# Kernel optimization log

Hardware: AMD Instinct MI355X
Metric: run time of the kernel (lower is better)

## Reference

```python
import jax, jax.numpy as jnp
import numpy as np

BLOCK_SIZE = 16
# Signed NVFP4 (e2m1) value table; code = sign_bit<<3 | magnitude_index
FP4_VALUES = jnp.array(
    [0.0, 0.5, 1.0, 1.5, 2.0, 3.0, 4.0, 6.0,
     -0.0, -0.5, -1.0, -1.5, -2.0, -3.0, -4.0, -6.0],
    dtype=jnp.float32)


def setup_inputs() -> dict:
    key = jax.random.key(0)
    k1, k2, k3 = jax.random.split(key, 3)
    O, I = 4096, 4096
    x = jax.random.normal(k1, (2, 1024, I), dtype=jnp.float32)
    # per-block scales (positive), one per 16-element block along in_features
    weight_scales = jax.random.uniform(k2, (O, I // BLOCK_SIZE), dtype=jnp.float32,
                                       minval=0.01, maxval=1.0)
    weight_q = jax.random.randint(k3, (O, I), 0, 16, dtype=jnp.int32)
    return {"x": x, "weight_scales": weight_scales, "weight_q": weight_q}


def dequantize_nvfp4_sim(weight_q, weight_scales, block_size=BLOCK_SIZE):
    O, I = weight_q.shape
    vals = FP4_VALUES[weight_q]                              # [O, I] fp32 e2m1 values
    w = vals.reshape(O, I // block_size, block_size) * weight_scales[:, :, None]
    return w.reshape(O, I)


def reference(x, weight_scales, weight_q):
    # Dequantize NVFP4 -> BF16, then BF16 GEMM (F.linear), cast back to input dtype.
    w = dequantize_nvfp4_sim(weight_q, weight_scales).astype(jnp.bfloat16)  # [O, I]
    x_bf16 = x.astype(jnp.bfloat16)
    out = jnp.einsum('bsi,oi->bso', x_bf16, w)               # [B, S, O] bf16
    return out.astype(x.dtype)
```

## Files before the change

kernel.cpp:

```cpp
#include <hip/hip_runtime.h>

typedef __bf16  bf16x8 __attribute__((ext_vector_type(8)));
typedef float   f32x4  __attribute__((ext_vector_type(4)));
typedef short   short8 __attribute__((ext_vector_type(8)));

static __device__ __forceinline__ unsigned short f2bf(float f) {
  union { float f; unsigned int u; } v; v.f = f;
  unsigned int u = v.u;
  u += 0x7fffu + ((u >> 16) & 1u);
  return (unsigned short)(u >> 16);
}

static __device__ __forceinline__ float fp4_decode(int qc) {
  int e = (qc >> 1) & 3;
  float m = (float)(qc & 1);
  float mag = (e == 0) ? (0.5f * m)
                       : ((2.0f + m) * 0.5f * (float)(1 << (e - 1)));
  return (qc & 8) ? -mag : mag;
}

__global__ __launch_bounds__(256) void w4a16_dequant_w(
    const int* __restrict__ wq, const float* __restrict__ wsc,
    short* __restrict__ wout, int nblk) {
  int idx = blockIdx.x * 256 + threadIdx.x;
  if (idx >= nblk) return;
  float s = wsc[idx];
  const int4* qp = (const int4*)wq + (size_t)idx * 4;
  int4 q0 = qp[0], q1 = qp[1], q2 = qp[2], q3 = qp[3];
  short8 r0, r1;
  r0[0] = (short)f2bf(fp4_decode(q0.x) * s);
  r0[1] = (short)f2bf(fp4_decode(q0.y) * s);
  r0[2] = (short)f2bf(fp4_decode(q0.z) * s);
  r0[3] = (short)f2bf(fp4_decode(q0.w) * s);
  r0[4] = (short)f2bf(fp4_decode(q1.x) * s);
  r0[5] = (short)f2bf(fp4_decode(q1.y) * s);
  r0[6] = (short)f2bf(fp4_decode(q1.z) * s);
  r0[7] = (short)f2bf(fp4_decode(q1.w) * s);
  r1[0] = (short)f2bf(fp4_decode(q2.x) * s);
  r1[1] = (short)f2bf(fp4_decode(q2.y) * s);
  r1[2] = (short)f2bf(fp4_decode(q2.z) * s);
  r1[3] = (short)f2bf(fp4_decode(q2.w) * s);
  r1[4] = (short)f2bf(fp4_decode(q3.x) * s);
  r1[5] = (short)f2bf(fp4_decode(q3.y) * s);
  r1[6] = (short)f2bf(fp4_decode(q3.z) * s);
  r1[7] = (short)f2bf(fp4_decode(q3.w) * s);
  short8* op = (short8*)wout + (size_t)idx * 2;
  op[0] = r0;
  op[1] = r1;
}

__global__ __launch_bounds__(256) void w4a16_convert_x(
    const float* __restrict__ x, short* __restrict__ xb, int n8) {
  int idx = blockIdx.x * 256 + threadIdx.x;
  if (idx >= n8) return;
  const float4* xp = (const float4*)x + (size_t)idx * 2;
  float4 a = xp[0], b = xp[1];
  short8 r;
  r[0] = (short)f2bf(a.x); r[1] = (short)f2bf(a.y);
  r[2] = (short)f2bf(a.z); r[3] = (short)f2bf(a.w);
  r[4] = (short)f2bf(b.x); r[5] = (short)f2bf(b.y);
  r[6] = (short)f2bf(b.z); r[7] = (short)f2bf(b.w);
  ((short8*)xb)[idx] = r;
}

#define BM 128
#define BN 256
#define BK 64
#define NBUF 3
#define ASZ (BM * BK)
#define BSZ (BN * BK)

__global__ __launch_bounds__(512, 2) void w4a16_gemm_2ph(
    const short* __restrict__ A, const short* __restrict__ B,
    float* __restrict__ C, int M, int N, int K) {
  __shared__ __attribute__((aligned(16))) short As[NBUF * ASZ];
  __shared__ __attribute__((aligned(16))) short Bs[NBUF * BSZ];

  const int tid  = threadIdx.x;
  const int lane = tid & 63;
  const int wid  = tid >> 6;
  const int wr   = wid >> 2;
  const int wc   = wid & 3;

  const int bm = blockIdx.y * BM;
  const int bn = blockIdx.x * BN;

  f32x4 acc[4][4] = {};

  const int fr    = lane & 15;
  const int klane = lane >> 4;
  const int xv    = fr & 7;

  const size_t rowbytes = (size_t)K * 2;

  size_t aoff[2];  int aldso[2];
#pragma unroll
  for (int r = 0; r < 2; ++r) {
    int u = r * 512 + tid;
    int row = u >> 3, c = u & 7;
    int csrc = c ^ (row & 7);
    aoff[r]  = (size_t)(bm + row) * rowbytes + (size_t)csrc * 16;
    aldso[r] = u * 16;
  }
  size_t boff[4];  int bldso[4];
#pragma unroll
  for (int r = 0; r < 4; ++r) {
    int u = r * 512 + tid;
    int row = u >> 3, c = u & 7;
    int csrc = c ^ (row & 7);
    boff[r]  = (size_t)(bn + row) * rowbytes + (size_t)csrc * 16;
    bldso[r] = u * 16;
  }

  const char* Ag = (const char*)A;
  const char* Bg = (const char*)B;

#define STAGE_A(bufbase, koff2, r)                                              \
  __builtin_amdgcn_global_load_lds(                                             \
      (const __attribute__((address_space(1))) unsigned int*)(Ag + aoff[r] + (koff2)), \
      (__attribute__((address_space(3))) unsigned int*)((char*)(bufbase) + aldso[r]),  \
      16, 0, 0)
#define STAGE_B(bufbase, koff2, r)                                              \
  __builtin_amdgcn_global_load_lds(                                             \
      (const __attribute__((address_space(1))) unsigned int*)(Bg + boff[r] + (koff2)), \
      (__attribute__((address_space(3))) unsigned int*)((char*)(bufbase) + bldso[r]),  \
      16, 0, 0)

  auto readA = [&](const short* Ab, int mq, int mi, int kk) -> bf16x8 {
    int row = wr * 64 + mq * 32 + mi * 16 + fr;
    int c = kk * 4 + klane;
    return *(const bf16x8*)((const char*)Ab + (size_t)row * 128 + ((c ^ xv) << 4));
  };
  auto readB = [&](const short* Bb, int ni, int kk) -> bf16x8 {
    int row = wc * 64 + ni * 16 + fr;
    int c = kk * 4 + klane;
    return *(const bf16x8*)((const char*)Bb + (size_t)row * 128 + ((c ^ xv) << 4));
  };

  const int NT = K / BK;

  {
    char* A0 = (char*)As; char* B0 = (char*)Bs;
    char* A1 = (char*)(As + ASZ); char* B1 = (char*)(Bs + BSZ);
    STAGE_A(A0, 0, 0); STAGE_A(A0, 0, 1);
    STAGE_B(B0, 0, 0); STAGE_B(B0, 0, 1); STAGE_B(B0, 0, 2); STAGE_B(B0, 0, 3);
    size_t k2 = (size_t)BK * 2;
    STAGE_A(A1, k2, 0); STAGE_A(A1, k2, 1);
    STAGE_B(B1, k2, 0); STAGE_B(B1, k2, 1); STAGE_B(B1, k2, 2); STAGE_B(B1, k2, 3);
  }
  asm volatile("s_waitcnt vmcnt(6)");
  __builtin_amdgcn_s_barrier();

  int cur = 0, nxt = 2;
  for (int t = 0; t < NT; ++t) {
    const short* Ab = As + cur * ASZ;
    const short* Bb = Bs + cur * BSZ;
    char* An = (char*)(As + nxt * ASZ);
    char* Bn = (char*)(Bs + nxt * BSZ);
    const size_t koff2 = (size_t)(t + 2) * (BK * 2);
    const bool pf = (t + 2) < NT;

    bf16x8 af[2][2], bfr[4][2];

#pragma unroll
    for (int mi = 0; mi < 2; ++mi)
#pragma unroll
      for (int kk = 0; kk < 2; ++kk)
        af[mi][kk] = readA(Ab, 0, mi, kk);
#pragma unroll
    for (int ni = 0; ni < 4; ++ni)
#pragma unroll
      for (int kk = 0; kk < 2; ++kk)
        bfr[ni][kk] = readB(Bb, ni, kk);

    if (pf) { STAGE_A(An, koff2, 0); STAGE_A(An, koff2, 1); STAGE_B(Bn, koff2, 0); }

    __builtin_amdgcn_s_barrier();
    asm volatile("s_waitcnt lgkmcnt(0)");
    __builtin_amdgcn_s_setprio(1);
#pragma unroll
    for (int mi = 0; mi < 2; ++mi)
#pragma unroll
      for (int ni = 0; ni < 4; ++ni)
#pragma unroll
        for (int kk = 0; kk < 2; ++kk)
          acc[mi][ni] = __builtin_amdgcn_mfma_f32_16x16x32_bf16(
              af[mi][kk], bfr[ni][kk], acc[mi][ni], 0, 0, 0);
    __builtin_amdgcn_s_setprio(0);
    __builtin_amdgcn_s_barrier();

#pragma unroll
    for (int mi = 0; mi < 2; ++mi)
#pragma unroll
      for (int kk = 0; kk < 2; ++kk)
        af[mi][kk] = readA(Ab, 1, mi, kk);

    if (pf) { STAGE_B(Bn, koff2, 1); STAGE_B(Bn, koff2, 2); STAGE_B(Bn, koff2, 3); }

    __builtin_amdgcn_s_barrier();
    asm volatile("s_waitcnt lgkmcnt(0)");
    __builtin_amdgcn_s_setprio(1);
#pragma unroll
    for (int mi = 0; mi < 2; ++mi)
#pragma unroll
      for (int ni = 0; ni < 4; ++ni)
#pragma unroll
        for (int kk = 0; kk < 2; ++kk)
          acc[2 + mi][ni] = __builtin_amdgcn_mfma_f32_16x16x32_bf16(
              af[mi][kk], bfr[ni][kk], acc[2 + mi][ni], 0, 0, 0);
    __builtin_amdgcn_s_setprio(0);

    if (t < NT - 1) {
      if (pf) asm volatile("s_waitcnt vmcnt(6)");
      else    asm volatile("s_waitcnt vmcnt(0)");
    }
    __builtin_amdgcn_s_barrier();

    cur = (cur == NBUF - 1) ? 0 : cur + 1;
    nxt = (nxt == NBUF - 1) ? 0 : nxt + 1;
  }

  const int cn = lane & 15;
  const int rb = (lane >> 4) * 4;
#pragma unroll
  for (int ai = 0; ai < 4; ++ai)
#pragma unroll
    for (int bj = 0; bj < 4; ++bj) {
      int m0 = bm + wr * 64 + ai * 16 + rb;
      int n0 = bn + wc * 64 + bj * 16 + cn;
#pragma unroll
      for (int r = 0; r < 4; ++r)
        C[(size_t)(m0 + r) * N + n0] = acc[ai][bj][r];
    }
}

extern "C" void kernel_launch(void* const* d_in, const int* in_sizes, int n_in,
                              void* d_out, int out_size, void* d_ws, size_t ws_size,
                              hipStream_t stream) {
  const float* x   = (const float*)d_in[0];
  const float* wsc = (const float*)d_in[1];
  const int*   wq  = (const int*)d_in[2];
  float* out = (float*)d_out;

  const int K = 4096;
  const int N = in_sizes[2] / K;
  const int M = in_sizes[0] / K;

  short* Wb = (short*)d_ws;
  short* Xb = Wb + (size_t)N * K;

  int nblk = (N * K) / 16;
  w4a16_dequant_w<<<nblk / 256, 256, 0, stream>>>(wq, wsc, Wb, nblk);
  int n8 = (M * K) / 8;
  w4a16_convert_x<<<n8 / 256, 256, 0, stream>>>(x, Xb, n8);

  dim3 grid(N / BN, M / BM);
  w4a16_gemm_2ph<<<grid, 512, 0, stream>>>(Xb, Wb, out, M, N, K);
}
```

Baseline: 97.93 us.

## Merge prep kernels and collapse GEMM inner loop into one phase

The weight-dequant and activation-convert kernels become a single launch that splits its blocks by index range, removing one launch and the gap between kernels. In the GEMM, the two half-iteration phases are merged: all A and B fragments for the tile are read from LDS up front, all six prefetch loads are issued together, and the two intermediate barriers and lgkmcnt waits are dropped, leaving one barrier per K step. This cuts synchronisation overhead but raises register pressure from the extra A fragments. It also relies on the triple-buffer distance and the end-of-iteration barrier to keep LDS reads and writes from racing.

New measurement: 90.93 us. -7.2%, faster.

```diff
diff --git a/kernel.cpp b/kernel.cpp
--- a/kernel.cpp
+++ b/kernel.cpp
@@ -19,48 +19,49 @@
   return (qc & 8) ? -mag : mag;
 }
 
-__global__ __launch_bounds__(256) void w4a16_dequant_w(
+__global__ __launch_bounds__(256) void w4a16_prep(
     const int* __restrict__ wq, const float* __restrict__ wsc,
-    short* __restrict__ wout, int nblk) {
-  int idx = blockIdx.x * 256 + threadIdx.x;
-  if (idx >= nblk) return;
-  float s = wsc[idx];
-  const int4* qp = (const int4*)wq + (size_t)idx * 4;
-  int4 q0 = qp[0], q1 = qp[1], q2 = qp[2], q3 = qp[3];
-  short8 r0, r1;
-  r0[0] = (short)f2bf(fp4_decode(q0.x) * s);
-  r0[1] = (short)f2bf(fp4_decode(q0.y) * s);
-  r0[2] = (short)f2bf(fp4_decode(q0.z) * s);
-  r0[3] = (short)f2bf(fp4_decode(q0.w) * s);
-  r0[4] = (short)f2bf(fp4_decode(q1.x) * s);
-  r0[5] = (short)f2bf(fp4_decode(q1.y) * s);
-  r0[6] = (short)f2bf(fp4_decode(q1.z) * s);
-  r0[7] = (short)f2bf(fp4_decode(q1.w) * s);
-  r1[0] = (short)f2bf(fp4_decode(q2.x) * s);
-  r1[1] = (short)f2bf(fp4_decode(q2.y) * s);
-  r1[2] = (short)f2bf(fp4_decode(q2.z) * s);
-  r1[3] = (short)f2bf(fp4_decode(q2.w) * s);
-  r1[4] = (short)f2bf(fp4_decode(q3.x) * s);
-  r1[5] = (short)f2bf(fp4_decode(q3.y) * s);
-  r1[6] = (short)f2bf(fp4_decode(q3.z) * s);
-  r1[7] = (short)f2bf(fp4_decode(q3.w) * s);
-  short8* op = (short8*)wout + (size_t)idx * 2;
-  op[0] = r0;
-  op[1] = r1;
-}
-
-__global__ __launch_bounds__(256) void w4a16_convert_x(
+    short* __restrict__ wout, int nblkW,
     const float* __restrict__ x, short* __restrict__ xb, int n8) {
-  int idx = blockIdx.x * 256 + threadIdx.x;
-  if (idx >= n8) return;
-  const float4* xp = (const float4*)x + (size_t)idx * 2;
-  float4 a = xp[0], b = xp[1];
-  short8 r;
-  r[0] = (short)f2bf(a.x); r[1] = (short)f2bf(a.y);
-  r[2] = (short)f2bf(a.z); r[3] = (short)f2bf(a.w);
-  r[4] = (short)f2bf(b.x); r[5] = (short)f2bf(b.y);
-  r[6] = (short)f2bf(b.z); r[7] = (short)f2bf(b.w);
-  ((short8*)xb)[idx] = r;
+  const int nbW = nblkW >> 8;
+  if ((int)blockIdx.x < nbW) {
+    int idx = blockIdx.x * 256 + threadIdx.x;
+    if (idx >= nblkW) return;
+    float s = wsc[idx];
+    const int4* qp = (const int4*)wq + (size_t)idx * 4;
+    int4 q0 = qp[0], q1 = qp[1], q2 = qp[2], q3 = qp[3];
+    short8 r0, r1;
+    r0[0] = (short)f2bf(fp4_decode(q0.x) * s);
+    r0[1] = (short)f2bf(fp4_decode(q0.y) * s);
+    r0[2] = (short)f2bf(fp4_decode(q0.z) * s);
+    r0[3] = (short)f2bf(fp4_decode(q0.w) * s);
+    r0[4] = (short)f2bf(fp4_decode(q1.x) * s);
+    r0[5] = (short)f2bf(fp4_decode(q1.y) * s);
+    r0[6] = (short)f2bf(fp4_decode(q1.z) * s);
+    r0[7] = (short)f2bf(fp4_decode(q1.w) * s);
+    r1[0] = (short)f2bf(fp4_decode(q2.x) * s);
+    r1[1] = (short)f2bf(fp4_decode(q2.y) * s);
+    r1[2] = (short)f2bf(fp4_decode(q2.z) * s);
+    r1[3] = (short)f2bf(fp4_decode(q2.w) * s);
+    r1[4] = (short)f2bf(fp4_decode(q3.x) * s);
+    r1[5] = (short)f2bf(fp4_decode(q3.y) * s);
+    r1[6] = (short)f2bf(fp4_decode(q3.z) * s);
+    r1[7] = (short)f2bf(fp4_decode(q3.w) * s);
+    short8* op = (short8*)wout + (size_t)idx * 2;
+    op[0] = r0;
+    op[1] = r1;
+  } else {
+    int idx = (blockIdx.x - nbW) * 256 + threadIdx.x;
+    if (idx >= n8) return;
+    const float4* xp = (const float4*)x + (size_t)idx * 2;
+    float4 a = xp[0], b = xp[1];
+    short8 r;
+    r[0] = (short)f2bf(a.x); r[1] = (short)f2bf(a.y);
+    r[2] = (short)f2bf(a.z); r[3] = (short)f2bf(a.w);
+    r[4] = (short)f2bf(b.x); r[5] = (short)f2bf(b.y);
+    r[6] = (short)f2bf(b.z); r[7] = (short)f2bf(b.w);
+    ((short8*)xb)[idx] = r;
+  }
 }
 
 #define BM 128
@@ -70,7 +71,7 @@
 #define ASZ (BM * BK)
 #define BSZ (BN * BK)
 
-__global__ __launch_bounds__(512, 2) void w4a16_gemm_2ph(
+__global__ __launch_bounds__(512, 2) void w4a16_gemm_1ph(
     const short* __restrict__ A, const short* __restrict__ B,
     float* __restrict__ C, int M, int N, int K) {
   __shared__ __attribute__((aligned(16))) short As[NBUF * ASZ];
@@ -160,23 +161,30 @@
     const size_t koff2 = (size_t)(t + 2) * (BK * 2);
     const bool pf = (t + 2) < NT;
 
-    bf16x8 af[2][2], bfr[4][2];
+    bf16x8 af0[2][2], bfr[4][2], af1[2][2];
 
 #pragma unroll
     for (int mi = 0; mi < 2; ++mi)
 #pragma unroll
       for (int kk = 0; kk < 2; ++kk)
-        af[mi][kk] = readA(Ab, 0, mi, kk);
+        af0[mi][kk] = readA(Ab, 0, mi, kk);
 #pragma unroll
     for (int ni = 0; ni < 4; ++ni)
 #pragma unroll
       for (int kk = 0; kk < 2; ++kk)
         bfr[ni][kk] = readB(Bb, ni, kk);
-
-    if (pf) { STAGE_A(An, koff2, 0); STAGE_A(An, koff2, 1); STAGE_B(Bn, koff2, 0); }
-
-    __builtin_amdgcn_s_barrier();
-    asm volatile("s_waitcnt lgkmcnt(0)");
+#pragma unroll
+    for (int mi = 0; mi < 2; ++mi)
+#pragma unroll
+      for (int kk = 0; kk < 2; ++kk)
+        af1[mi][kk] = readA(Ab, 1, mi, kk);
+
+    if (pf) {
+      STAGE_A(An, koff2, 0); STAGE_A(An, koff2, 1);
+      STAGE_B(Bn, koff2, 0); STAGE_B(Bn, koff2, 1);
+      STAGE_B(Bn, koff2, 2); STAGE_B(Bn, koff2, 3);
+    }
+
     __builtin_amdgcn_s_setprio(1);
 #pragma unroll
     for (int mi = 0; mi < 2; ++mi)
@@ -185,21 +193,7 @@
 #pragma unroll
         for (int kk = 0; kk < 2; ++kk)
           acc[mi][ni] = __builtin_amdgcn_mfma_f32_16x16x32_bf16(
-              af[mi][kk], bfr[ni][kk], acc[mi][ni], 0, 0, 0);
-    __builtin_amdgcn_s_setprio(0);
-    __builtin_amdgcn_s_barrier();
-
-#pragma unroll
-    for (int mi = 0; mi < 2; ++mi)
-#pragma unroll
-      for (int kk = 0; kk < 2; ++kk)
-        af[mi][kk] = readA(Ab, 1, mi, kk);
-
-    if (pf) { STAGE_B(Bn, koff2, 1); STAGE_B(Bn, koff2, 2); STAGE_B(Bn, koff2, 3); }
-
-    __builtin_amdgcn_s_barrier();
-    asm volatile("s_waitcnt lgkmcnt(0)");
-    __builtin_amdgcn_s_setprio(1);
+              af0[mi][kk], bfr[ni][kk], acc[mi][ni], 0, 0, 0);
 #pragma unroll
     for (int mi = 0; mi < 2; ++mi)
 #pragma unroll
@@ -207,10 +201,11 @@
 #pragma unroll
         for (int kk = 0; kk < 2; ++kk)
           acc[2 + mi][ni] = __builtin_amdgcn_mfma_f32_16x16x32_bf16(
-              af[mi][kk], bfr[ni][kk], acc[2 + mi][ni], 0, 0, 0);
+              af1[mi][kk], bfr[ni][kk], acc[2 + mi][ni], 0, 0, 0);
     __builtin_amdgcn_s_setprio(0);
 
     if (t < NT - 1) {
+      __builtin_amdgcn_sched_barrier(0);
       if (pf) asm volatile("s_waitcnt vmcnt(6)");
       else    asm volatile("s_waitcnt vmcnt(0)");
     }
@@ -249,11 +244,11 @@
   short* Wb = (short*)d_ws;
   short* Xb = Wb + (size_t)N * K;
 
-  int nblk = (N * K) / 16;
-  w4a16_dequant_w<<<nblk / 256, 256, 0, stream>>>(wq, wsc, Wb, nblk);
-  int n8 = (M * K) / 8;
-  w4a16_convert_x<<<n8 / 256, 256, 0, stream>>>(x, Xb, n8);
+  int nblkW = (N * K) / 16;
+  int n8    = (M * K) / 8;
+  int gridP = (nblkW >> 8) + ((n8 + 255) >> 8);
+  w4a16_prep<<<gridP, 256, 0, stream>>>(wq, wsc, Wb, nblkW, x, Xb, n8);
 
   dim3 grid(N / BN, M / BM);
-  w4a16_gemm_2ph<<<grid, 512, 0, stream>>>(Xb, Wb, out, M, N, K);
-}
+  w4a16_gemm_1ph<<<grid, 512, 0, stream>>>(Xb, Wb, out, M, N, K);
+}
```
